# Optimization experiments

Measured on AMD Instinct MI355X. Metric: run time of the kernel, lower is better.

Reference implementation:

```python
import jax, jax.numpy as jnp
import numpy as np

KH, KW = 3, 3
PAD = (1, 1, 1, 1)  # torch F.pad order: (W_left, W_right, H_top, H_bottom)
STRIDE = 1
B, CIN, COUT, H, W = 4, 32, 32, 128, 128


def setup_inputs() -> dict:
    key = jax.random.key(0)
    k1, k2, k3, k4 = jax.random.split(key, 4)
    f = jax.random.normal(k1, (B, CIN, H, W), jnp.float32)
    # orientation field components (cos/sin of a random angle field)
    theta = jax.random.uniform(k2, (B, CIN, H, W), jnp.float32, 0.0, 2.0 * np.pi)
    r0 = jnp.cos(theta)
    r1 = jnp.sin(theta)
    # learned conv weight (nn.Conv2d default uniform init, no bias)
    fan_in = CIN * KH * KW
    bound = 1.0 / np.sqrt(fan_in)
    w = jax.random.uniform(k3, (COUT, CIN, KH, KW), jnp.float32, -bound, bound)
    # frozen wr: (randn * pi * 100) / a with a = 100  ->  randn * pi
    wr = jax.random.normal(k4, (COUT, CIN, KH, KW), jnp.float32) * np.pi
    return {"f": f, "r0": r0, "r1": r1, "w": w, "wr": wr}


def _rot90(w):
    # torch: w.permute(0,1,2,4,3).flip([4]) on the (kh,kw) dims
    return jnp.flip(jnp.swapaxes(w, -1, -2), -1)


def _conv_single(f, r0, r1, w, wr):
    # f, r0, r1: (B, Cin, Hp, Wp);  w, wr: (Cout, Cin, KH, KW)
    Hp, Wp = f.shape[2], f.shape[3]
    he = Hp - PAD[0] - PAD[1]
    we = Wp - PAD[2] - PAD[3]
    s = STRIDE
    out = None
    for i in range(KH):
        for j in range(KW):
            fw = f[:, :, i:i + he:s, j:j + we:s]    # (B, Cin, h, w)
            r0w = r0[:, :, i:i + he:s, j:j + we:s]
            r1w = r1[:, :, i:i + he:s, j:j + we:s]
            c = jnp.cos(wr[:, :, i, j])[None, :, :, None, None]   # (1, Cout, Cin, 1, 1)
            sn = jnp.sin(wr[:, :, i, j])[None, :, :, None, None]
            # lambda_theta: relu of orientation-projected field, (B, Cout, Cin, h, w)
            lam = jax.nn.relu(c * r0w[:, None] + sn * r1w[:, None])
            term = jnp.einsum('bchw,oc,bochw->bohw', fw, w[:, :, i, j], lam)
            out = term if out is None else out + term
    return out  # (B, Cout, h, w)


def _forward(f, r0, r1, w, wr):
    pl, pr, pt, pb = PAD
    pad = ((0, 0), (0, 0), (pt, pb), (pl, pr))
    fp = jnp.pad(f, pad)
    r0p = jnp.pad(r0, pad)
    r1p = jnp.pad(r1, pad)
    orient = jnp.arange(4, dtype=f.dtype) * jnp.asarray(np.pi / 2, f.dtype)
    outs = []
    wk = w
    for o in range(4):
        if o > 0:
            wk = _rot90(wk)
        outs.append(_conv_single(fp, r0p, r1p, wk, wr + orient[o]))
    stacked = jnp.stack(outs, axis=2)              # (B, Cout, 4, h, w)
    idx = jnp.argmax(stacked, axis=2)              # (B, Cout, h, w)
    out = jnp.take_along_axis(stacked, idx[:, :, None], axis=2)[:, :, 0]
    out_r = orient[idx]                            # winning orientation angle
    return out, jnp.cos(out_r), jnp.sin(out_r)


def reference(f, r0, r1, w, wr):
    return _forward(f, r0, r1, w, wr)
```

## Files before the change

### kernel.cpp

```cpp
#include <hip/hip_runtime.h>


typedef float v2f __attribute__((ext_vector_type(2)));

#define B_    4
#define CIN_  32
#define COUT_ 32
#define H_    128
#define W_    128
#define OUTSZ_ (B_ * COUT_ * H_ * W_)

__global__ __launch_bounds__(256, 4)
void orient_conv_kernel(const float* __restrict__ f,
                        const float* __restrict__ r0,
                        const float* __restrict__ r1,
                        const float* __restrict__ w,
                        const float* __restrict__ wr,
                        float* __restrict__ out)
{
    __shared__ float sIn[3][3][68];
    __shared__ float sW[9][32][12];

    const int tid   = threadIdx.x;
    const int bid   = blockIdx.x;
    const int b     = bid >> 8;
    const int rem   = bid & 255;
    const int h     = rem >> 1;
    const int wbase = (rem & 1) << 6;
    const int px0   = tid & 31;
    const int oc0   = (tid >> 5) << 2;

    v2f acc[4][4];
#pragma unroll
    for (int q = 0; q < 4; ++q)
#pragma unroll
        for (int o = 0; o < 4; ++o) acc[q][o] = (v2f)(0.0f);

    for (int c = 0; c < CIN_; ++c) {
        if (tid < 198) {
            int row = tid / 66;
            int col = tid - row * 66;
            int gh = h + row - 1;
            int gw = wbase + col - 1;
            bool ok = ((unsigned)gh < (unsigned)H_) & ((unsigned)gw < (unsigned)W_);
            int off = ((b * CIN_ + c) * H_ + gh) * W_ + gw;
            sIn[0][row][col] = ok ? f[off]  : 0.0f;
            sIn[1][row][col] = ok ? r0[off] : 0.0f;
            sIn[2][row][col] = ok ? r1[off] : 0.0f;
        }
        for (int idx = tid; idx < 288; idx += 256) {
            int oc  = idx & 31;
            int tap = idx >> 5;
            int i = tap / 3;
            int j = tap - i * 3;
            const int base = (oc * CIN_ + c) * 9;
            float wv0 = w[base + i * 3 + j];
            float wv1 = w[base + (2 - j) * 3 + i];
            float wv2 = w[base + (2 - i) * 3 + (2 - j)];
            float wv3 = w[base + j * 3 + (2 - i)];
            float S, C;
            sincosf(wr[base + i * 3 + j], &S, &C);
            float4* dst = reinterpret_cast<float4*>(&sW[tap][oc][0]);
            dst[0] = make_float4(C, C, S, S);
            dst[1] = make_float4(wv0, wv0, wv1, wv1);
            dst[2] = make_float4(wv2, wv2, wv3, wv3);
        }
        __syncthreads();

#pragma unroll
        for (int tap = 0; tap < 9; ++tap) {
            const int i = tap / 3;
            const int j = tap - i * 3;
            const int colb = px0 + j;
            v2f fv, r0v, r1v;
            fv[0]  = sIn[0][i][colb]; fv[1]  = sIn[0][i][colb + 32];
            r0v[0] = sIn[1][i][colb]; r0v[1] = sIn[1][i][colb + 32];
            r1v[0] = sIn[2][i][colb]; r1v[1] = sIn[2][i][colb + 32];
#pragma unroll
            for (int q = 0; q < 4; ++q) {
                const float4 wcs = *reinterpret_cast<const float4*>(&sW[tap][oc0 + q][0]);
                const float4 w01 = *reinterpret_cast<const float4*>(&sW[tap][oc0 + q][4]);
                const float4 w23 = *reinterpret_cast<const float4*>(&sW[tap][oc0 + q][8]);
                v2f Cv; Cv[0] = wcs.x; Cv[1] = wcs.y;
                v2f Sv; Sv[0] = wcs.z; Sv[1] = wcs.w;
                v2f w0v; w0v[0] = w01.x; w0v[1] = w01.y;
                v2f w1v; w1v[0] = w01.z; w1v[1] = w01.w;
                v2f w2v; w2v[0] = w23.x; w2v[1] = w23.y;
                v2f w3v; w3v[0] = w23.z; w3v[1] = w23.w;

                v2f u  = __builtin_elementwise_fma(Cv, r0v, Sv * r1v);
                v2f vv = __builtin_elementwise_fma(Cv, r1v, -Sv * r0v);
                v2f g0 = __builtin_elementwise_max(u,  (v2f)(0.0f));
                v2f g1 = __builtin_elementwise_max(vv, (v2f)(0.0f));
                v2f g2 = g0 - u;
                v2f g3 = g1 - vv;
                v2f t0 = fv * g0, t1 = fv * g1, t2 = fv * g2, t3 = fv * g3;
                acc[q][0] = __builtin_elementwise_fma(t0, w0v, acc[q][0]);
                acc[q][1] = __builtin_elementwise_fma(t1, w1v, acc[q][1]);
                acc[q][2] = __builtin_elementwise_fma(t2, w2v, acc[q][2]);
                acc[q][3] = __builtin_elementwise_fma(t3, w3v, acc[q][3]);
            }
        }
        __syncthreads();
    }

    const float cosv[4] = {1.0f, -4.37113883e-08f, -1.0f, 1.19248806e-08f};
    const float sinv[4] = {0.0f, 1.0f, -8.74227766e-08f, -1.0f};
#pragma unroll
    for (int q = 0; q < 4; ++q) {
        int oc = oc0 + q;
#pragma unroll
        for (int k = 0; k < 2; ++k) {
            int wcol = wbase + px0 + (k << 5);
            float a0 = acc[q][0][k], a1 = acc[q][1][k];
            float a2 = acc[q][2][k], a3 = acc[q][3][k];
            float best = a0; int bi = 0;
            if (a1 > best) { best = a1; bi = 1; }
            if (a2 > best) { best = a2; bi = 2; }
            if (a3 > best) { best = a3; bi = 3; }
            size_t o = ((size_t)(b * COUT_ + oc) * H_ + h) * W_ + wcol;
            out[o]              = best;
            out[o + OUTSZ_]     = cosv[bi];
            out[o + 2 * OUTSZ_] = sinv[bi];
        }
    }
}

extern "C" void kernel_launch(void* const* d_in, const int* in_sizes, int n_in,
                              void* d_out, int out_size, void* d_ws, size_t ws_size,
                              hipStream_t stream)
{
    const float* f  = (const float*)d_in[0];
    const float* r0 = (const float*)d_in[1];
    const float* r1 = (const float*)d_in[2];
    const float* w  = (const float*)d_in[3];
    const float* wr = (const float*)d_in[4];
    float* out = (float*)d_out;

    dim3 grid(B_ * H_ * 2);
    dim3 block(256);
    orient_conv_kernel<<<grid, block, 0, stream>>>(f, r0, r1, w, wr, out);
}
```

Measured before the change: 329.7 us.

## Precompute weight/sincos table once and make weights wave-uniform scalar loads

A small pre-kernel builds a global table holding cos/sin of wr and the four rotated weights per (cin, output-channel group, tap), so the per-block, per-channel sincos and LDS weight staging are removed. The main kernel is remapped so each wavefront owns 8 output channels across 64 pixels. Weight reads then depend only on the wave index and can become scalar loads, while the rotation math is packed across channel pairs instead of pixel pairs. This adds a second launch and a workspace buffer, and the number of LDS reads of input values per useful FMA changes.

```diff
diff --git a/kernel.cpp b/kernel.cpp
--- a/kernel.cpp
+++ b/kernel.cpp
@@ -10,31 +10,60 @@
 #define W_    128
 #define OUTSZ_ (B_ * COUT_ * H_ * W_)
 
+#define TAB_FLOATS (CIN_ * 4 * 9 * 4 * 12)
+
+__global__ __launch_bounds__(256)
+void build_wtab(const float* __restrict__ w, const float* __restrict__ wr,
+                float* __restrict__ tab)
+{
+    int idx = blockIdx.x * 256 + threadIdx.x;
+    if (idx >= CIN_ * 4 * 9 * 4 * 2) return;
+    int k    = idx & 1;
+    int r    = idx >> 1;
+    int pair = r & 3;
+    int r2   = r >> 2;
+    int tap  = r2 % 9;
+    int t2   = r2 / 9;
+    int ocg  = t2 & 3;
+    int c    = t2 >> 2;
+    int oc   = ocg * 8 + pair * 2 + k;
+    int i = tap / 3, j = tap - i * 3;
+    int base = (oc * CIN_ + c) * 9;
+    float w0 = w[base + i * 3 + j];
+    float w1 = w[base + (2 - j) * 3 + i];
+    float w2 = w[base + (2 - i) * 3 + (2 - j)];
+    float w3 = w[base + j * 3 + (2 - i)];
+    float S, C;
+    sincosf(wr[base + i * 3 + j], &S, &C);
+    float* dst = tab + ((size_t)t2 * 9 + tap) * 48 + pair * 12;
+    dst[0 + k]  = C;  dst[2 + k]  = S;
+    dst[4 + k]  = w0; dst[6 + k]  = w1;
+    dst[8 + k]  = w2; dst[10 + k] = w3;
+}
+
 __global__ __launch_bounds__(256, 4)
 void orient_conv_kernel(const float* __restrict__ f,
                         const float* __restrict__ r0,
                         const float* __restrict__ r1,
-                        const float* __restrict__ w,
-                        const float* __restrict__ wr,
+                        const float* __restrict__ tab,
                         float* __restrict__ out)
 {
     __shared__ float sIn[3][3][68];
-    __shared__ float sW[9][32][12];
 
     const int tid   = threadIdx.x;
+    const int lane  = tid & 63;
+    const int ocg   = __builtin_amdgcn_readfirstlane(tid >> 6);
     const int bid   = blockIdx.x;
     const int b     = bid >> 8;
     const int rem   = bid & 255;
     const int h     = rem >> 1;
     const int wbase = (rem & 1) << 6;
-    const int px0   = tid & 31;
-    const int oc0   = (tid >> 5) << 2;
 
     v2f acc[4][4];
 #pragma unroll
-    for (int q = 0; q < 4; ++q)
+    for (int p = 0; p < 4; ++p)
 #pragma unroll
-        for (int o = 0; o < 4; ++o) acc[q][o] = (v2f)(0.0f);
+        for (int o = 0; o < 4; ++o) acc[p][o] = (v2f)(0.0f);
 
     for (int c = 0; c < CIN_; ++c) {
         if (tid < 198) {
@@ -48,57 +77,37 @@
             sIn[1][row][col] = ok ? r0[off] : 0.0f;
             sIn[2][row][col] = ok ? r1[off] : 0.0f;
         }
-        for (int idx = tid; idx < 288; idx += 256) {
-            int oc  = idx & 31;
-            int tap = idx >> 5;
-            int i = tap / 3;
-            int j = tap - i * 3;
-            const int base = (oc * CIN_ + c) * 9;
-            float wv0 = w[base + i * 3 + j];
-            float wv1 = w[base + (2 - j) * 3 + i];
-            float wv2 = w[base + (2 - i) * 3 + (2 - j)];
-            float wv3 = w[base + j * 3 + (2 - i)];
-            float S, C;
-            sincosf(wr[base + i * 3 + j], &S, &C);
-            float4* dst = reinterpret_cast<float4*>(&sW[tap][oc][0]);
-            dst[0] = make_float4(C, C, S, S);
-            dst[1] = make_float4(wv0, wv0, wv1, wv1);
-            dst[2] = make_float4(wv2, wv2, wv3, wv3);
-        }
         __syncthreads();
+
+        const float* wt = tab + ((size_t)(c * 4 + ocg) * 9) * 48;
 
 #pragma unroll
         for (int tap = 0; tap < 9; ++tap) {
             const int i = tap / 3;
             const int j = tap - i * 3;
-            const int colb = px0 + j;
-            v2f fv, r0v, r1v;
-            fv[0]  = sIn[0][i][colb]; fv[1]  = sIn[0][i][colb + 32];
-            r0v[0] = sIn[1][i][colb]; r0v[1] = sIn[1][i][colb + 32];
-            r1v[0] = sIn[2][i][colb]; r1v[1] = sIn[2][i][colb + 32];
+            const int col = lane + j;
+            float fv  = sIn[0][i][col];
+            float r0s = sIn[1][i][col];
+            float r1s = sIn[2][i][col];
+            v2f fd;  fd[0]  = fv;  fd[1]  = fv;
+            v2f r0d; r0d[0] = r0s; r0d[1] = r0s;
+            v2f r1d; r1d[0] = r1s; r1d[1] = r1s;
+            const float* wp = wt + tap * 48;
 #pragma unroll
-            for (int q = 0; q < 4; ++q) {
-                const float4 wcs = *reinterpret_cast<const float4*>(&sW[tap][oc0 + q][0]);
-                const float4 w01 = *reinterpret_cast<const float4*>(&sW[tap][oc0 + q][4]);
-                const float4 w23 = *reinterpret_cast<const float4*>(&sW[tap][oc0 + q][8]);
-                v2f Cv; Cv[0] = wcs.x; Cv[1] = wcs.y;
-                v2f Sv; Sv[0] = wcs.z; Sv[1] = wcs.w;
-                v2f w0v; w0v[0] = w01.x; w0v[1] = w01.y;
-                v2f w1v; w1v[0] = w01.z; w1v[1] = w01.w;
-                v2f w2v; w2v[0] = w23.x; w2v[1] = w23.y;
-                v2f w3v; w3v[0] = w23.z; w3v[1] = w23.w;
-
-                v2f u  = __builtin_elementwise_fma(Cv, r0v, Sv * r1v);
-                v2f vv = __builtin_elementwise_fma(Cv, r1v, -Sv * r0v);
+            for (int p = 0; p < 4; ++p) {
+                const v2f* q = reinterpret_cast<const v2f*>(wp + p * 12);
+                v2f Cv = q[0], Sv = q[1];
+                v2f w0 = q[2], w1 = q[3], w2 = q[4], w3 = q[5];
+                v2f u  = __builtin_elementwise_fma(Cv, r0d, Sv * r1d);
+                v2f vv = __builtin_elementwise_fma(Cv, r1d, -(Sv * r0d));
                 v2f g0 = __builtin_elementwise_max(u,  (v2f)(0.0f));
                 v2f g1 = __builtin_elementwise_max(vv, (v2f)(0.0f));
                 v2f g2 = g0 - u;
                 v2f g3 = g1 - vv;
-                v2f t0 = fv * g0, t1 = fv * g1, t2 = fv * g2, t3 = fv * g3;
-                acc[q][0] = __builtin_elementwise_fma(t0, w0v, acc[q][0]);
-                acc[q][1] = __builtin_elementwise_fma(t1, w1v, acc[q][1]);
-                acc[q][2] = __builtin_elementwise_fma(t2, w2v, acc[q][2]);
-                acc[q][3] = __builtin_elementwise_fma(t3, w3v, acc[q][3]);
+                acc[p][0] = __builtin_elementwise_fma(fd * g0, w0, acc[p][0]);
+                acc[p][1] = __builtin_elementwise_fma(fd * g1, w1, acc[p][1]);
+                acc[p][2] = __builtin_elementwise_fma(fd * g2, w2, acc[p][2]);
+                acc[p][3] = __builtin_elementwise_fma(fd * g3, w3, acc[p][3]);
             }
         }
         __syncthreads();
@@ -106,14 +115,14 @@
 
     const float cosv[4] = {1.0f, -4.37113883e-08f, -1.0f, 1.19248806e-08f};
     const float sinv[4] = {0.0f, 1.0f, -8.74227766e-08f, -1.0f};
+    const int wcol = wbase + lane;
 #pragma unroll
-    for (int q = 0; q < 4; ++q) {
-        int oc = oc0 + q;
+    for (int p = 0; p < 4; ++p) {
 #pragma unroll
         for (int k = 0; k < 2; ++k) {
-            int wcol = wbase + px0 + (k << 5);
-            float a0 = acc[q][0][k], a1 = acc[q][1][k];
-            float a2 = acc[q][2][k], a3 = acc[q][3][k];
+            int oc = ocg * 8 + p * 2 + k;
+            float a0 = acc[p][0][k], a1 = acc[p][1][k];
+            float a2 = acc[p][2][k], a3 = acc[p][3][k];
             float best = a0; int bi = 0;
             if (a1 > best) { best = a1; bi = 1; }
             if (a2 > best) { best = a2; bi = 2; }
@@ -136,8 +145,9 @@
     const float* w  = (const float*)d_in[3];
     const float* wr = (const float*)d_in[4];
     float* out = (float*)d_out;
+    float* tab = (float*)d_ws;
 
-    dim3 grid(B_ * H_ * 2);
-    dim3 block(256);
-    orient_conv_kernel<<<grid, block, 0, stream>>>(f, r0, r1, w, wr, out);
+    build_wtab<<<dim3(36), dim3(256), 0, stream>>>(w, wr, tab);
+    orient_conv_kernel<<<dim3(B_ * H_ * 2), dim3(256), 0, stream>>>(
+        f, r0, r1, tab, out);
 }
```

New measurement: 320.2 us. -2.9%, faster.
